# Performance work log

Measured on AMD Instinct MI355X. Metric: run time of the kernel, lower is better.

The kernel has to match this reference:

```python
import jax, jax.numpy as jnp
import numpy as np

KH, KW = 3, 3
STRIDE = 1
PAD = 1


def setup_inputs() -> dict:
    key = jax.random.key(0)
    kf, ko, kw_ = jax.random.split(key, 3)
    B, C, H, W = 4, 128, 96, 320
    Cout = 128
    features = jax.random.normal(kf, (B, C, H, W), dtype=jnp.float32)
    # perspective offsets in the original are O(offset_2d / D_RATIO) = O(2)
    offsets = jax.random.normal(ko, (B, 2 * KH * KW, H, W), dtype=jnp.float32) * 2.0
    weight = jax.random.normal(kw_, (Cout, C, KH, KW), dtype=jnp.float32) * (1.0 / np.sqrt(C * KH * KW))
    return {"features": features, "offsets": offsets, "weight": weight}


def _bilinear_sample(img, py, px):
    """img: [C,H,W]; py, px: [K,Ho,Wo] float sampling locations.
    Zero padding outside the image (torchvision deform_conv2d semantics).
    Returns [C,K,Ho,Wo]."""
    C, H, W = img.shape
    y0 = jnp.floor(py)
    x0 = jnp.floor(px)
    y1 = y0 + 1.0
    x1 = x0 + 1.0
    wy1 = py - y0
    wy0 = 1.0 - wy1
    wx1 = px - x0
    wx0 = 1.0 - wx1

    def gather(yy, xx):
        valid = (yy >= 0) & (yy <= H - 1) & (xx >= 0) & (xx <= W - 1)
        yi = jnp.clip(yy, 0, H - 1).astype(jnp.int32)
        xi = jnp.clip(xx, 0, W - 1).astype(jnp.int32)
        v = img[:, yi, xi]  # [C,K,Ho,Wo]
        return v * valid[None].astype(img.dtype)

    return (gather(y0, x0) * (wy0 * wx0)[None]
            + gather(y0, x1) * (wy0 * wx1)[None]
            + gather(y1, x0) * (wy1 * wx0)[None]
            + gather(y1, x1) * (wy1 * wx1)[None])


def deform_conv2d(x, offset, weight, stride=STRIDE, pad=PAD):
    B, C, H, W = x.shape
    Cout, Cin, kh, kw = weight.shape
    Ho = (H + 2 * pad - kh) // stride + 1
    Wo = (W + 2 * pad - kw) // stride + 1
    K = kh * kw
    # torchvision layout: channel 2k = dy, channel 2k+1 = dx, taps row-major
    off = offset.reshape(B, K, 2, Ho, Wo)
    ky, kx = jnp.meshgrid(jnp.arange(kh), jnp.arange(kw), indexing='ij')
    ky = ky.reshape(-1).astype(x.dtype)  # [K]
    kx = kx.reshape(-1).astype(x.dtype)
    hy = (jnp.arange(Ho) * stride - pad).astype(x.dtype)  # [Ho]
    wx = (jnp.arange(Wo) * stride - pad).astype(x.dtype)  # [Wo]
    base_y = ky[:, None, None] + hy[None, :, None]  # [K,Ho,1]
    base_x = kx[:, None, None] + wx[None, None, :]  # [K,1,Wo]
    py = base_y[None] + off[:, :, 0]  # [B,K,Ho,Wo]
    px = base_x[None] + off[:, :, 1]
    sampled = jax.vmap(_bilinear_sample)(x, py, px)  # [B,C,K,Ho,Wo]
    out = jnp.einsum('ok,bkn->bon',
                     weight.reshape(Cout, Cin * K),
                     sampled.reshape(B, Cin * K, Ho * Wo))
    return out.reshape(B, Cout, Ho, Wo)


def reference(features, offsets, weight):
    return deform_conv2d(features, offsets, weight)
```

## Files before the change

kernel.cpp:

```cpp
#include <hip/hip_runtime.h>
#include <hip/hip_fp16.h>

#define IH   96
#define IW   320
#define NB   4
#define CIN  128
#define COUT 128
#define NKP  9
#define HW   (IH*IW)

typedef float    f32x4 __attribute__((ext_vector_type(4)));
typedef _Float16 f16x8 __attribute__((ext_vector_type(8)));

__global__ __launch_bounds__(256) void k_transpose(const float* __restrict__ in,
                                                   unsigned* __restrict__ dst32) {
    __shared__ float tile[32][129];
    int bid = blockIdx.x;
    int xc = bid % 10;
    int by = bid / 10;
    int y = by % IH;
    int b = by / IH;
    int x0 = xc * 32;
    int tid = threadIdx.x;

    const float* src = in + (size_t)b * CIN * HW + (size_t)y * IW + x0;
#pragma unroll
    for (int i = 0; i < 16; ++i) {
        int idx = tid + 256 * i;
        int c = idx >> 5, xl = idx & 31;
        tile[xl][c] = src[(size_t)c * HW + xl];
    }
    __syncthreads();
    unsigned* d = dst32 + ((size_t)(b * IH + y) * IW + x0) * 64;
#pragma unroll
    for (int i = 0; i < 8; ++i) {
        int idx = tid + 256 * i;
        int c2 = idx & 63, xl = idx >> 6;
        __half2 p;
        p.x = __float2half(tile[xl][2 * c2]);
        p.y = __float2half(tile[xl][2 * c2 + 1]);
        d[xl * 64 + c2] = *(unsigned*)&p;
    }
}

__global__ __launch_bounds__(256) void k_prepack(const float* __restrict__ w,
                                                 _Float16* __restrict__ wb) {
    int idx = blockIdx.x * 256 + threadIdx.x;
    int kp = idx >> 14;
    int cout = (idx >> 7) & 127;
    int c = idx & 127;
    wb[idx] = (_Float16)w[(cout * CIN + c) * NKP + kp];
}

__global__ __launch_bounds__(256) void k_meta(const float* __restrict__ off,
                                              uint4* __restrict__ meta) {
    int idx = blockIdx.x * 256 + threadIdx.x;
    int wo = idx % IW;
    int t = idx / IW;
    int ho = t % IH;
    t /= IH;
    int kp = t % NKP;
    int b = t / NKP;

    float dy = off[((size_t)(b * 18 + 2 * kp) * IH + ho) * IW + wo];
    float dx = off[((size_t)(b * 18 + 2 * kp + 1) * IH + ho) * IW + wo];
    int ky = kp / 3, kx = kp - 3 * (kp / 3);
    float py = (float)(ho - 1 + ky) + dy;
    float px = (float)(wo - 1 + kx) + dx;
    float y0f = floorf(py), x0f = floorf(px);
    float wy1 = py - y0f, wx1 = px - x0f;
    float wy0 = 1.f - wy1, wx0 = 1.f - wx1;
    int y0 = (int)y0f, x0 = (int)x0f, y1 = y0 + 1, x1 = x0 + 1;
    wy0 = (y0 >= 0 && y0 < IH) ? wy0 : 0.f;
    wy1 = (y1 >= 0 && y1 < IH) ? wy1 : 0.f;
    wx0 = (x0 >= 0 && x0 < IW) ? wx0 : 0.f;
    wx1 = (x1 >= 0 && x1 < IW) ? wx1 : 0.f;
    int yc0 = min(max(y0, 0), IH - 1), yc1 = min(max(y1, 0), IH - 1);
    int xc0 = min(max(x0, 0), IW - 1), xc1 = min(max(x1, 0), IW - 1);
    unsigned r0 = (unsigned)((b * IH + yc0) * IW);
    unsigned r1 = (unsigned)((b * IH + yc1) * IW);

    auto pk = [](float w) {
        __half h = __float2half(w);
        __half2 p; p.x = h; p.y = h;
        return *(unsigned*)&p;
    };
    uint4 m0 = {pk(wy0 * wx0), pk(wy0 * wx1), pk(wy1 * wx0), pk(wy1 * wx1)};
    uint4 m1 = {(r0 + (unsigned)xc0) << 8, (r0 + (unsigned)xc1) << 8,
                (r1 + (unsigned)xc0) << 8, (r1 + (unsigned)xc1) << 8};
    meta[(size_t)idx * 2] = m0;
    meta[(size_t)idx * 2 + 1] = m1;
}

__global__ __launch_bounds__(256, 4) void k_main(const uint4* __restrict__ meta,
                                                 const char* __restrict__ fb,
                                                 const _Float16* __restrict__ wb,
                                                 float* __restrict__ out) {
    __shared__ unsigned colbuf[64 * 64];

    const int tid  = threadIdx.x;
    const int lane = tid & 63;
    const int wv   = tid >> 6;
    int bid = (blockIdx.x & 7) * 240 + (blockIdx.x >> 3);
    const int n0   = bid * 64;
    const int b    = n0 / HW;
    const int rem  = n0 - b * HW;
    const int ho   = rem / IW;
    const int wo0  = rem - ho * IW;
    const int lane4 = lane << 2;

    f32x4 acc[2][4];
#pragma unroll
    for (int mi = 0; mi < 2; ++mi)
#pragma unroll
        for (int nj = 0; nj < 4; ++nj)
            acc[mi][nj] = (f32x4){0.f, 0.f, 0.f, 0.f};

    for (int kp = 0; kp < NKP; ++kp) {
        const int itemBase = ((b * NKP + kp) * IH + ho) * IW + wo0;
#pragma unroll 4
        for (int i = 0; i < 16; ++i) {
            int p = (wv << 4) + i;
            int it = __builtin_amdgcn_readfirstlane(itemBase + p);
            uint4 mw = meta[(size_t)it * 2];
            uint4 ma = meta[(size_t)it * 2 + 1];
            __half2 u00 = *(const __half2*)(fb + ma.x + lane4);
            __half2 u01 = *(const __half2*)(fb + ma.y + lane4);
            __half2 u10 = *(const __half2*)(fb + ma.z + lane4);
            __half2 u11 = *(const __half2*)(fb + ma.w + lane4);
            __half2 s = __hmul2(*(const __half2*)&mw.x, u00);
            s = __hfma2(*(const __half2*)&mw.y, u01, s);
            s = __hfma2(*(const __half2*)&mw.z, u10, s);
            s = __hfma2(*(const __half2*)&mw.w, u11, s);
            colbuf[(p << 6) + (lane ^ ((p & 7) << 2))] = *(unsigned*)&s;
        }
        __syncthreads();

        const _Float16* wkbase =
            wb + (size_t)kp * COUT * CIN + (size_t)(wv * 32 + (lane & 15)) * CIN + 8 * (lane >> 4);
#pragma unroll
        for (int c0 = 0; c0 < CIN; c0 += 32) {
            f16x8 a0 = *(const f16x8*)(wkbase + c0);
            f16x8 a1 = *(const f16x8*)(wkbase + 16 * CIN + c0);
            int cb = (c0 >> 1) + 4 * (lane >> 4);
#pragma unroll
            for (int nj = 0; nj < 4; ++nj) {
                int pos = nj * 16 + (lane & 15);
                f16x8 bfr = *(const f16x8*)(&colbuf[(pos << 6) + (cb ^ ((pos & 7) << 2))]);
                acc[0][nj] = __builtin_amdgcn_mfma_f32_16x16x32_f16(a0, bfr, acc[0][nj], 0, 0, 0);
                acc[1][nj] = __builtin_amdgcn_mfma_f32_16x16x32_f16(a1, bfr, acc[1][nj], 0, 0, 0);
            }
        }
        __syncthreads();
    }

#pragma unroll
    for (int mi = 0; mi < 2; ++mi) {
#pragma unroll
        for (int nj = 0; nj < 4; ++nj) {
            int cout = wv * 32 + mi * 16 + ((lane >> 4) << 2);
            int wo = wo0 + nj * 16 + (lane & 15);
            float* op = out + ((size_t)(b * COUT + cout) * IH + ho) * IW + wo;
#pragma unroll
            for (int r = 0; r < 4; ++r)
                op[(size_t)r * HW] = acc[mi][nj][r];
        }
    }
}

extern "C" void kernel_launch(void* const* d_in, const int* in_sizes, int n_in,
                              void* d_out, int out_size, void* d_ws, size_t ws_size,
                              hipStream_t stream) {
    const float* features = (const float*)d_in[0];
    const float* offsets  = (const float*)d_in[1];
    const float* weight   = (const float*)d_in[2];
    float* out = (float*)d_out;

    unsigned*  nhwc = (unsigned*)d_ws;
    _Float16*  wbuf = (_Float16*)((char*)d_ws + (size_t)NB * HW * CIN * 2);
    uint4*     meta = (uint4*)((char*)d_ws + (size_t)NB * HW * CIN * 2 + 294912);

    hipLaunchKernelGGL(k_transpose, dim3(NB * IH * (IW / 32)), dim3(256), 0, stream, features, nhwc);
    hipLaunchKernelGGL(k_prepack, dim3(576), dim3(256), 0, stream, weight, wbuf);
    hipLaunchKernelGGL(k_meta, dim3(NB * NKP * IH * IW / 256), dim3(256), 0, stream, offsets, meta);
    hipLaunchKernelGGL(k_main, dim3((NB * HW) / 64), dim3(256), 0, stream,
                       meta, (const char*)nhwc, wbuf, out);
}
```

Baseline: 249.2 us.

## Double-buffer im2col gather against MFMA and merge preprocessing kernels

Merges the transpose, weight prepack and meta kernels into one launch that dispatches on block index. The main kernel gains a double-buffered LDS column buffer, so the bilinear gather for the next kernel tap is issued and interleaved with the MFMAs on the current tap, with one barrier per tap instead of two. Each block now handles two 64-pixel tiles in sequence, and the weights for a tap are loaded into registers up front. This is meant to hide gather latency and cut launch overhead, at the cost of more LDS and more registers, which may lower occupancy.

```diff
diff --git a/kernel.cpp b/kernel.cpp
--- a/kernel.cpp
+++ b/kernel.cpp
@@ -12,49 +12,53 @@
 typedef float    f32x4 __attribute__((ext_vector_type(4)));
 typedef _Float16 f16x8 __attribute__((ext_vector_type(8)));
 
-__global__ __launch_bounds__(256) void k_transpose(const float* __restrict__ in,
-                                                   unsigned* __restrict__ dst32) {
+__global__ __launch_bounds__(256) void k_pre(const float* __restrict__ feat,
+                                             const float* __restrict__ off,
+                                             const float* __restrict__ w,
+                                             unsigned* __restrict__ nhwc,
+                                             _Float16* __restrict__ wb,
+                                             uint4* __restrict__ meta) {
     __shared__ float tile[32][129];
     int bid = blockIdx.x;
-    int xc = bid % 10;
-    int by = bid / 10;
-    int y = by % IH;
-    int b = by / IH;
-    int x0 = xc * 32;
     int tid = threadIdx.x;
 
-    const float* src = in + (size_t)b * CIN * HW + (size_t)y * IW + x0;
-#pragma unroll
-    for (int i = 0; i < 16; ++i) {
-        int idx = tid + 256 * i;
-        int c = idx >> 5, xl = idx & 31;
-        tile[xl][c] = src[(size_t)c * HW + xl];
+    if (bid < 3840) {
+        int xc = bid % 10;
+        int by = bid / 10;
+        int y = by % IH;
+        int b = by / IH;
+        int x0 = xc * 32;
+        const float* src = feat + (size_t)b * CIN * HW + (size_t)y * IW + x0;
+#pragma unroll
+        for (int i = 0; i < 16; ++i) {
+            int idx = tid + 256 * i;
+            int c = idx >> 5, xl = idx & 31;
+            tile[xl][c] = src[(size_t)c * HW + xl];
+        }
+        __syncthreads();
+        unsigned* d = nhwc + ((size_t)(b * IH + y) * IW + x0) * 64;
+#pragma unroll
+        for (int i = 0; i < 8; ++i) {
+            int idx = tid + 256 * i;
+            int c2 = idx & 63, xl = idx >> 6;
+            __half2 p;
+            p.x = __float2half(tile[xl][2 * c2]);
+            p.y = __float2half(tile[xl][2 * c2 + 1]);
+            d[xl * 64 + c2] = *(unsigned*)&p;
+        }
+        return;
     }
-    __syncthreads();
-    unsigned* d = dst32 + ((size_t)(b * IH + y) * IW + x0) * 64;
-#pragma unroll
-    for (int i = 0; i < 8; ++i) {
-        int idx = tid + 256 * i;
-        int c2 = idx & 63, xl = idx >> 6;
-        __half2 p;
-        p.x = __float2half(tile[xl][2 * c2]);
-        p.y = __float2half(tile[xl][2 * c2 + 1]);
-        d[xl * 64 + c2] = *(unsigned*)&p;
+    bid -= 3840;
+    if (bid < 576) {
+        int idx = bid * 256 + tid;
+        int kp = idx >> 14;
+        int cout = (idx >> 7) & 127;
+        int c = idx & 127;
+        wb[idx] = (_Float16)w[(cout * CIN + c) * NKP + kp];
+        return;
     }
-}
-
-__global__ __launch_bounds__(256) void k_prepack(const float* __restrict__ w,
-                                                 _Float16* __restrict__ wb) {
-    int idx = blockIdx.x * 256 + threadIdx.x;
-    int kp = idx >> 14;
-    int cout = (idx >> 7) & 127;
-    int c = idx & 127;
-    wb[idx] = (_Float16)w[(cout * CIN + c) * NKP + kp];
-}
-
-__global__ __launch_bounds__(256) void k_meta(const float* __restrict__ off,
-                                              uint4* __restrict__ meta) {
-    int idx = blockIdx.x * 256 + threadIdx.x;
+    bid -= 576;
+    int idx = bid * 256 + tid;
     int wo = idx % IW;
     int t = idx / IW;
     int ho = t % IH;
@@ -79,9 +83,8 @@
     int xc0 = min(max(x0, 0), IW - 1), xc1 = min(max(x1, 0), IW - 1);
     unsigned r0 = (unsigned)((b * IH + yc0) * IW);
     unsigned r1 = (unsigned)((b * IH + yc1) * IW);
-
-    auto pk = [](float w) {
-        __half h = __float2half(w);
+    auto pk = [](float wgt) {
+        __half h = __float2half(wgt);
         __half2 p; p.x = h; p.y = h;
         return *(unsigned*)&p;
     };
@@ -96,74 +99,127 @@
                                                  const char* __restrict__ fb,
                                                  const _Float16* __restrict__ wb,
                                                  float* __restrict__ out) {
-    __shared__ unsigned colbuf[64 * 64];
+    __shared__ unsigned colbuf[2 * 64 * 64];
+    char* cb_ = (char*)colbuf;
 
     const int tid  = threadIdx.x;
     const int lane = tid & 63;
     const int wv   = tid >> 6;
-    int bid = (blockIdx.x & 7) * 240 + (blockIdx.x >> 3);
-    const int n0   = bid * 64;
-    const int b    = n0 / HW;
-    const int rem  = n0 - b * HW;
-    const int ho   = rem / IW;
-    const int wo0  = rem - ho * IW;
-    const int lane4 = lane << 2;
-
-    f32x4 acc[2][4];
-#pragma unroll
-    for (int mi = 0; mi < 2; ++mi)
-#pragma unroll
-        for (int nj = 0; nj < 4; ++nj)
-            acc[mi][nj] = (f32x4){0.f, 0.f, 0.f, 0.f};
-
-    for (int kp = 0; kp < NKP; ++kp) {
-        const int itemBase = ((b * NKP + kp) * IH + ho) * IW + wo0;
-#pragma unroll 4
-        for (int i = 0; i < 16; ++i) {
-            int p = (wv << 4) + i;
-            int it = __builtin_amdgcn_readfirstlane(itemBase + p);
-            uint4 mw = meta[(size_t)it * 2];
-            uint4 ma = meta[(size_t)it * 2 + 1];
-            __half2 u00 = *(const __half2*)(fb + ma.x + lane4);
-            __half2 u01 = *(const __half2*)(fb + ma.y + lane4);
-            __half2 u10 = *(const __half2*)(fb + ma.z + lane4);
-            __half2 u11 = *(const __half2*)(fb + ma.w + lane4);
-            __half2 s = __hmul2(*(const __half2*)&mw.x, u00);
-            s = __hfma2(*(const __half2*)&mw.y, u01, s);
-            s = __hfma2(*(const __half2*)&mw.z, u10, s);
-            s = __hfma2(*(const __half2*)&mw.w, u11, s);
-            colbuf[(p << 6) + (lane ^ ((p & 7) << 2))] = *(unsigned*)&s;
+    const int posl = lane & 15;
+    const int hi   = lane >> 4;
+    const int x    = (posl & 7) << 2;
+    const int vA   = (posl << 8) + (((4 * hi) ^ (x & 12)) << 2);
+    const int xe   = (x & 16) << 2;
+    const int xo   = xe ^ 64;
+    const int l4   = lane << 2;
+    const int wrb0 = l4 + (wv << 12);
+
+    int bid = (blockIdx.x & 7) * 120 + (blockIdx.x >> 3);
+    const int n0 = bid * 128;
+    const int b  = n0 / HW;
+    const int nrem0 = n0 - b * HW;
+
+    const int wvoff = (wv * 32 + posl) * CIN + 8 * hi;
+
+    for (int st = 0; st < 2; ++st) {
+        const int nrem = nrem0 + st * 64;
+        f32x4 acc[2][4];
+#pragma unroll
+        for (int mi = 0; mi < 2; ++mi)
+#pragma unroll
+            for (int nj = 0; nj < 4; ++nj)
+                acc[mi][nj] = (f32x4){0.f, 0.f, 0.f, 0.f};
+
+        {
+            const int itBase = (b * NKP + 0) * HW + nrem + wv * 16;
+#pragma unroll
+            for (int i = 0; i < 16; ++i) {
+                int it = __builtin_amdgcn_readfirstlane(itBase + i);
+                uint4 mw = meta[(size_t)it * 2];
+                uint4 ma = meta[(size_t)it * 2 + 1];
+                unsigned u0 = *(const unsigned*)(fb + ma.x + l4);
+                unsigned u1 = *(const unsigned*)(fb + ma.y + l4);
+                unsigned u2 = *(const unsigned*)(fb + ma.z + l4);
+                unsigned u3 = *(const unsigned*)(fb + ma.w + l4);
+                __half2 s = __hmul2(*(const __half2*)&mw.x, *(const __half2*)&u0);
+                s = __hfma2(*(const __half2*)&mw.y, *(const __half2*)&u1, s);
+                s = __hfma2(*(const __half2*)&mw.z, *(const __half2*)&u2, s);
+                s = __hfma2(*(const __half2*)&mw.w, *(const __half2*)&u3, s);
+                *(unsigned*)(cb_ + (wrb0 ^ ((i & 7) << 4)) + (i << 8)) = *(unsigned*)&s;
+            }
         }
         __syncthreads();
 
-        const _Float16* wkbase =
-            wb + (size_t)kp * COUT * CIN + (size_t)(wv * 32 + (lane & 15)) * CIN + 8 * (lane >> 4);
-#pragma unroll
-        for (int c0 = 0; c0 < CIN; c0 += 32) {
-            f16x8 a0 = *(const f16x8*)(wkbase + c0);
-            f16x8 a1 = *(const f16x8*)(wkbase + 16 * CIN + c0);
-            int cb = (c0 >> 1) + 4 * (lane >> 4);
+        for (int kp = 0; kp < NKP; ++kp) {
+            const int cur = kp & 1;
+            const int curB = cur << 14;
+            const int nxtB = curB ^ (1 << 14);
+            const int ave = vA + xe + curB;
+            const int avo = vA + xo + curB;
+            const int wrb = wrb0 + nxtB;
+            const int itBase = (b * NKP + (kp + 1)) * HW + nrem + wv * 16;
+            const bool more = (kp < NKP - 1);
+
+            const _Float16* wk0 = wb + (size_t)kp * COUT * CIN + wvoff;
+            const _Float16* wk1 = wk0 + 16 * CIN;
+            f16x8 wl[2][4];
+#pragma unroll
+            for (int g = 0; g < 4; ++g) {
+                wl[0][g] = *(const f16x8*)(wk0 + 32 * g);
+                wl[1][g] = *(const f16x8*)(wk1 + 32 * g);
+            }
+
+#pragma unroll
+            for (int q = 0; q < 4; ++q) {
+                uint4 mwv[4];
+                unsigned ug[4][4];
+                if (more) {
+#pragma unroll
+                    for (int i = 0; i < 4; ++i) {
+                        int it = __builtin_amdgcn_readfirstlane(itBase + q * 4 + i);
+                        mwv[i] = meta[(size_t)it * 2];
+                        uint4 ma = meta[(size_t)it * 2 + 1];
+                        ug[i][0] = *(const unsigned*)(fb + ma.x + l4);
+                        ug[i][1] = *(const unsigned*)(fb + ma.y + l4);
+                        ug[i][2] = *(const unsigned*)(fb + ma.z + l4);
+                        ug[i][3] = *(const unsigned*)(fb + ma.w + l4);
+                    }
+                }
+                {
+                    const int sel = (q & 1) ? avo : ave;
+                    const int himm = (q >> 1) << 7;
+#pragma unroll
+                    for (int nj = 0; nj < 4; ++nj) {
+                        f16x8 bf = *(const f16x8*)(cb_ + sel + ((nj << 12) + himm));
+                        acc[0][nj] = __builtin_amdgcn_mfma_f32_16x16x32_f16(wl[0][q], bf, acc[0][nj], 0, 0, 0);
+                        acc[1][nj] = __builtin_amdgcn_mfma_f32_16x16x32_f16(wl[1][q], bf, acc[1][nj], 0, 0, 0);
+                    }
+                }
+                if (more) {
+#pragma unroll
+                    for (int i = 0; i < 4; ++i) {
+                        __half2 s = __hmul2(*(const __half2*)&mwv[i].x, *(const __half2*)&ug[i][0]);
+                        s = __hfma2(*(const __half2*)&mwv[i].y, *(const __half2*)&ug[i][1], s);
+                        s = __hfma2(*(const __half2*)&mwv[i].z, *(const __half2*)&ug[i][2], s);
+                        s = __hfma2(*(const __half2*)&mwv[i].w, *(const __half2*)&ug[i][3], s);
+                        const int p = q * 4 + i;
+                        *(unsigned*)(cb_ + (wrb ^ ((p & 7) << 4)) + (p << 8)) = *(unsigned*)&s;
+                    }
+                }
+            }
+            __syncthreads();
+        }
+
+        float* obase = out + ((size_t)(b * COUT + wv * 32)) * HW + nrem;
+#pragma unroll
+        for (int mi = 0; mi < 2; ++mi) {
 #pragma unroll
             for (int nj = 0; nj < 4; ++nj) {
-                int pos = nj * 16 + (lane & 15);
-                f16x8 bfr = *(const f16x8*)(&colbuf[(pos << 6) + (cb ^ ((pos & 7) << 2))]);
-                acc[0][nj] = __builtin_amdgcn_mfma_f32_16x16x32_f16(a0, bfr, acc[0][nj], 0, 0, 0);
-                acc[1][nj] = __builtin_amdgcn_mfma_f32_16x16x32_f16(a1, bfr, acc[1][nj], 0, 0, 0);
-            }
-        }
-        __syncthreads();
-    }
-
-#pragma unroll
-    for (int mi = 0; mi < 2; ++mi) {
-#pragma unroll
-        for (int nj = 0; nj < 4; ++nj) {
-            int cout = wv * 32 + mi * 16 + ((lane >> 4) << 2);
-            int wo = wo0 + nj * 16 + (lane & 15);
-            float* op = out + ((size_t)(b * COUT + cout) * IH + ho) * IW + wo;
-#pragma unroll
-            for (int r = 0; r < 4; ++r)
-                op[(size_t)r * HW] = acc[mi][nj][r];
+                float* op = obase + (size_t)(mi * 16 + 4 * hi) * HW + nj * 16 + posl;
+#pragma unroll
+                for (int r = 0; r < 4; ++r)
+                    op[(size_t)r * HW] = acc[mi][nj][r];
+            }
         }
     }
 }
@@ -180,9 +236,8 @@
     _Float16*  wbuf = (_Float16*)((char*)d_ws + (size_t)NB * HW * CIN * 2);
     uint4*     meta = (uint4*)((char*)d_ws + (size_t)NB * HW * CIN * 2 + 294912);
 
-    hipLaunchKernelGGL(k_transpose, dim3(NB * IH * (IW / 32)), dim3(256), 0, stream, features, nhwc);
-    hipLaunchKernelGGL(k_prepack, dim3(576), dim3(256), 0, stream, weight, wbuf);
-    hipLaunchKernelGGL(k_meta, dim3(NB * NKP * IH * IW / 256), dim3(256), 0, stream, offsets, meta);
-    hipLaunchKernelGGL(k_main, dim3((NB * HW) / 64), dim3(256), 0, stream,
+    hipLaunchKernelGGL(k_pre, dim3(8736), dim3(256), 0, stream,
+                       features, offsets, weight, nhwc, wbuf, meta);
+    hipLaunchKernelGGL(k_main, dim3(960), dim3(256), 0, stream,
                        meta, (const char*)nhwc, wbuf, out);
 }
```

After: 268.7 us. 1.08x slower.

## Fuse sampling metadata into main kernel and merge transpose with weight prepack

Applied to the files above, without the earlier changes.

Removes the separate metadata kernel and its global buffer. Each block now computes bilinear indices and weights for its 64 positions directly from the offsets, double-buffered in shared memory and overlapped with the gather of the previous tap. The transpose and weight-prepack kernels are merged into one launch, and the metadata is packed more compactly (x1 encoded as a one-bit delta, fp16 weight pairs splatted at use). Occupancy hint rises to 6 blocks per SM. This cuts launches and global metadata traffic in exchange for extra ALU work and a partially idle wave inside the main kernel.

```diff
diff --git a/kernel.cpp b/kernel.cpp
--- a/kernel.cpp
+++ b/kernel.cpp
@@ -12,102 +12,103 @@
 typedef float    f32x4 __attribute__((ext_vector_type(4)));
 typedef _Float16 f16x8 __attribute__((ext_vector_type(8)));
 
-__global__ __launch_bounds__(256) void k_transpose(const float* __restrict__ in,
-                                                   unsigned* __restrict__ dst32) {
+__device__ __forceinline__ unsigned splat_lo(unsigned u) { return (u & 0xffffu) | (u << 16); }
+__device__ __forceinline__ unsigned splat_hi(unsigned u) { return (u >> 16) | (u & 0xffff0000u); }
+
+__global__ __launch_bounds__(256) void k_pre(const float* __restrict__ feat,
+                                             const float* __restrict__ w,
+                                             unsigned* __restrict__ nhwc,
+                                             _Float16* __restrict__ wb) {
     __shared__ float tile[32][129];
     int bid = blockIdx.x;
-    int xc = bid % 10;
-    int by = bid / 10;
-    int y = by % IH;
-    int b = by / IH;
-    int x0 = xc * 32;
     int tid = threadIdx.x;
 
-    const float* src = in + (size_t)b * CIN * HW + (size_t)y * IW + x0;
+    if (bid < 3840) {
+        int xc = bid % 10;
+        int by = bid / 10;
+        int y = by % IH;
+        int b = by / IH;
+        int x0 = xc * 32;
+        const float* src = feat + (size_t)b * CIN * HW + (size_t)y * IW + x0;
 #pragma unroll
-    for (int i = 0; i < 16; ++i) {
-        int idx = tid + 256 * i;
-        int c = idx >> 5, xl = idx & 31;
-        tile[xl][c] = src[(size_t)c * HW + xl];
+        for (int i = 0; i < 16; ++i) {
+            int idx = tid + 256 * i;
+            int c = idx >> 5, xl = idx & 31;
+            tile[xl][c] = src[(size_t)c * HW + xl];
+        }
+        __syncthreads();
+        unsigned* d = nhwc + ((size_t)(b * IH + y) * IW + x0) * 64;
+#pragma unroll
+        for (int i = 0; i < 8; ++i) {
+            int idx = tid + 256 * i;
+            int c2 = idx & 63, xl = idx >> 6;
+            __half2 p;
+            p.x = __float2half(tile[xl][2 * c2]);
+            p.y = __float2half(tile[xl][2 * c2 + 1]);
+            d[xl * 64 + c2] = *(unsigned*)&p;
+        }
+        return;
     }
-    __syncthreads();
-    unsigned* d = dst32 + ((size_t)(b * IH + y) * IW + x0) * 64;
-#pragma unroll
-    for (int i = 0; i < 8; ++i) {
-        int idx = tid + 256 * i;
-        int c2 = idx & 63, xl = idx >> 6;
-        __half2 p;
-        p.x = __float2half(tile[xl][2 * c2]);
-        p.y = __float2half(tile[xl][2 * c2 + 1]);
-        d[xl * 64 + c2] = *(unsigned*)&p;
-    }
-}
-
-__global__ __launch_bounds__(256) void k_prepack(const float* __restrict__ w,
-                                                 _Float16* __restrict__ wb) {
-    int idx = blockIdx.x * 256 + threadIdx.x;
+    bid -= 3840;
+    int idx = bid * 256 + tid;
     int kp = idx >> 14;
     int cout = (idx >> 7) & 127;
     int c = idx & 127;
     wb[idx] = (_Float16)w[(cout * CIN + c) * NKP + kp];
 }
 
-__global__ __launch_bounds__(256) void k_meta(const float* __restrict__ off,
-                                              uint4* __restrict__ meta) {
-    int idx = blockIdx.x * 256 + threadIdx.x;
-    int wo = idx % IW;
-    int t = idx / IW;
-    int ho = t % IH;
-    t /= IH;
-    int kp = t % NKP;
-    int b = t / NKP;
-
-    float dy = off[((size_t)(b * 18 + 2 * kp) * IH + ho) * IW + wo];
-    float dx = off[((size_t)(b * 18 + 2 * kp + 1) * IH + ho) * IW + wo];
-    int ky = kp / 3, kx = kp - 3 * (kp / 3);
-    float py = (float)(ho - 1 + ky) + dy;
-    float px = (float)(wo - 1 + kx) + dx;
-    float y0f = floorf(py), x0f = floorf(px);
-    float wy1 = py - y0f, wx1 = px - x0f;
-    float wy0 = 1.f - wy1, wx0 = 1.f - wx1;
-    int y0 = (int)y0f, x0 = (int)x0f, y1 = y0 + 1, x1 = x0 + 1;
-    wy0 = (y0 >= 0 && y0 < IH) ? wy0 : 0.f;
-    wy1 = (y1 >= 0 && y1 < IH) ? wy1 : 0.f;
-    wx0 = (x0 >= 0 && x0 < IW) ? wx0 : 0.f;
-    wx1 = (x1 >= 0 && x1 < IW) ? wx1 : 0.f;
-    int yc0 = min(max(y0, 0), IH - 1), yc1 = min(max(y1, 0), IH - 1);
-    int xc0 = min(max(x0, 0), IW - 1), xc1 = min(max(x1, 0), IW - 1);
-    unsigned r0 = (unsigned)((b * IH + yc0) * IW);
-    unsigned r1 = (unsigned)((b * IH + yc1) * IW);
-
-    auto pk = [](float w) {
-        __half h = __float2half(w);
-        __half2 p; p.x = h; p.y = h;
-        return *(unsigned*)&p;
-    };
-    uint4 m0 = {pk(wy0 * wx0), pk(wy0 * wx1), pk(wy1 * wx0), pk(wy1 * wx1)};
-    uint4 m1 = {(r0 + (unsigned)xc0) << 8, (r0 + (unsigned)xc1) << 8,
-                (r1 + (unsigned)xc0) << 8, (r1 + (unsigned)xc1) << 8};
-    meta[(size_t)idx * 2] = m0;
-    meta[(size_t)idx * 2 + 1] = m1;
-}
-
-__global__ __launch_bounds__(256, 4) void k_main(const uint4* __restrict__ meta,
+__global__ __launch_bounds__(256, 6) void k_main(const float* __restrict__ off,
                                                  const char* __restrict__ fb,
                                                  const _Float16* __restrict__ wb,
                                                  float* __restrict__ out) {
     __shared__ unsigned colbuf[64 * 64];
+    __shared__ uint4 metabuf[2][64];
 
     const int tid  = threadIdx.x;
     const int lane = tid & 63;
     const int wv   = tid >> 6;
+    const int posl = lane & 15;
+    const int hi   = lane >> 4;
+    const int l4   = lane << 2;
+
     int bid = (blockIdx.x & 7) * 240 + (blockIdx.x >> 3);
-    const int n0   = bid * 64;
-    const int b    = n0 / HW;
-    const int rem  = n0 - b * HW;
-    const int ho   = rem / IW;
-    const int wo0  = rem - ho * IW;
-    const int lane4 = lane << 2;
+    const int n0  = bid * 64;
+    const int b   = n0 / HW;
+    const int rem = n0 - b * HW;
+    const int ho  = rem / IW;
+    const int wo0 = rem - ho * IW;
+
+    const bool mlane = (lane < 16);
+    const int mp = wv * 16 + posl;
+    const int rowoff = ho * IW + wo0 + mp;
+
+    auto metacalc = [&](int k) {
+        if (!mlane) return;
+        const float* basep = off + (size_t)(b * 18 + 2 * k) * HW + rowoff;
+        float dy = basep[0];
+        float dx = basep[HW];
+        int ky = k / 3, kx = k - 3 * (k / 3);
+        float py = (float)(ho - 1 + ky) + dy;
+        float px = (float)(wo0 + mp - 1 + kx) + dx;
+        float y0f = floorf(py), x0f = floorf(px);
+        float wy1 = py - y0f, wx1 = px - x0f;
+        float wy0 = 1.f - wy1, wx0 = 1.f - wx1;
+        int y0 = (int)y0f, x0 = (int)x0f, y1 = y0 + 1, x1 = x0 + 1;
+        wy0 = (y0 >= 0 && y0 < IH) ? wy0 : 0.f;
+        wy1 = (y1 >= 0 && y1 < IH) ? wy1 : 0.f;
+        wx0 = (x0 >= 0 && x0 < IW) ? wx0 : 0.f;
+        wx1 = (x1 >= 0 && x1 < IW) ? wx1 : 0.f;
+        int yc0 = min(max(y0, 0), IH - 1), yc1 = min(max(y1, 0), IH - 1);
+        int xc0 = min(max(x0, 0), IW - 1), xc1 = min(max(x1, 0), IW - 1);
+        uint4 m;
+        m.x = ((unsigned)((b * IH + yc0) * IW + xc0) << 8) | (unsigned)(xc1 - xc0);
+        m.y = (unsigned)((b * IH + yc1) * IW + xc0) << 8;
+        __half2 wz; wz.x = __float2half(wy0 * wx0); wz.y = __float2half(wy0 * wx1);
+        __half2 ww; ww.x = __float2half(wy1 * wx0); ww.y = __float2half(wy1 * wx1);
+        m.z = *(unsigned*)&wz;
+        m.w = *(unsigned*)&ww;
+        metabuf[k & 1][mp] = m;
+    };
 
     f32x4 acc[2][4];
 #pragma unroll
@@ -116,36 +117,42 @@
         for (int nj = 0; nj < 4; ++nj)
             acc[mi][nj] = (f32x4){0.f, 0.f, 0.f, 0.f};
 
+    metacalc(0);
+    __syncthreads();
+
     for (int kp = 0; kp < NKP; ++kp) {
-        const int itemBase = ((b * NKP + kp) * IH + ho) * IW + wo0;
-#pragma unroll 4
+        const int cur = kp & 1;
+#pragma unroll
         for (int i = 0; i < 16; ++i) {
             int p = (wv << 4) + i;
-            int it = __builtin_amdgcn_readfirstlane(itemBase + p);
-            uint4 mw = meta[(size_t)it * 2];
-            uint4 ma = meta[(size_t)it * 2 + 1];
-            __half2 u00 = *(const __half2*)(fb + ma.x + lane4);
-            __half2 u01 = *(const __half2*)(fb + ma.y + lane4);
-            __half2 u10 = *(const __half2*)(fb + ma.z + lane4);
-            __half2 u11 = *(const __half2*)(fb + ma.w + lane4);
-            __half2 s = __hmul2(*(const __half2*)&mw.x, u00);
-            s = __hfma2(*(const __half2*)&mw.y, u01, s);
-            s = __hfma2(*(const __half2*)&mw.z, u10, s);
-            s = __hfma2(*(const __half2*)&mw.w, u11, s);
+            uint4 m = metabuf[cur][p];
+            unsigned d  = (m.x & 1u) << 8;
+            unsigned a00 = m.x & 0xffffff00u;
+            unsigned u00 = *(const unsigned*)(fb + a00 + l4);
+            unsigned u01 = *(const unsigned*)(fb + (a00 + d) + l4);
+            unsigned u10 = *(const unsigned*)(fb + m.y + l4);
+            unsigned u11 = *(const unsigned*)(fb + (m.y + d) + l4);
+            unsigned w00 = splat_lo(m.z), w01 = splat_hi(m.z);
+            unsigned w10 = splat_lo(m.w), w11 = splat_hi(m.w);
+            __half2 s = __hmul2(*(__half2*)&w00, *(__half2*)&u00);
+            s = __hfma2(*(__half2*)&w01, *(__half2*)&u01, s);
+            s = __hfma2(*(__half2*)&w10, *(__half2*)&u10, s);
+            s = __hfma2(*(__half2*)&w11, *(__half2*)&u11, s);
             colbuf[(p << 6) + (lane ^ ((p & 7) << 2))] = *(unsigned*)&s;
         }
+        if (kp < NKP - 1) metacalc(kp + 1);
         __syncthreads();
 
         const _Float16* wkbase =
-            wb + (size_t)kp * COUT * CIN + (size_t)(wv * 32 + (lane & 15)) * CIN + 8 * (lane >> 4);
+            wb + (size_t)kp * COUT * CIN + (size_t)(wv * 32 + posl) * CIN + 8 * hi;
 #pragma unroll
         for (int c0 = 0; c0 < CIN; c0 += 32) {
             f16x8 a0 = *(const f16x8*)(wkbase + c0);
             f16x8 a1 = *(const f16x8*)(wkbase + 16 * CIN + c0);
-            int cb = (c0 >> 1) + 4 * (lane >> 4);
+            int cb = (c0 >> 1) + 4 * hi;
 #pragma unroll
             for (int nj = 0; nj < 4; ++nj) {
-                int pos = nj * 16 + (lane & 15);
+                int pos = nj * 16 + posl;
                 f16x8 bfr = *(const f16x8*)(&colbuf[(pos << 6) + (cb ^ ((pos & 7) << 2))]);
                 acc[0][nj] = __builtin_amdgcn_mfma_f32_16x16x32_f16(a0, bfr, acc[0][nj], 0, 0, 0);
                 acc[1][nj] = __builtin_amdgcn_mfma_f32_16x16x32_f16(a1, bfr, acc[1][nj], 0, 0, 0);
@@ -158,8 +165,8 @@
     for (int mi = 0; mi < 2; ++mi) {
 #pragma unroll
         for (int nj = 0; nj < 4; ++nj) {
-            int cout = wv * 32 + mi * 16 + ((lane >> 4) << 2);
-            int wo = wo0 + nj * 16 + (lane & 15);
+            int cout = wv * 32 + mi * 16 + 4 * hi;
+            int wo = wo0 + nj * 16 + posl;
             float* op = out + ((size_t)(b * COUT + cout) * IH + ho) * IW + wo;
 #pragma unroll
             for (int r = 0; r < 4; ++r)
@@ -178,11 +185,9 @@
 
     unsigned*  nhwc = (unsigned*)d_ws;
     _Float16*  wbuf = (_Float16*)((char*)d_ws + (size_t)NB * HW * CIN * 2);
-    uint4*     meta = (uint4*)((char*)d_ws + (size_t)NB * HW * CIN * 2 + 294912);
 
-    hipLaunchKernelGGL(k_transpose, dim3(NB * IH * (IW / 32)), dim3(256), 0, stream, features, nhwc);
-    hipLaunchKernelGGL(k_prepack, dim3(576), dim3(256), 0, stream, weight, wbuf);
-    hipLaunchKernelGGL(k_meta, dim3(NB * NKP * IH * IW / 256), dim3(256), 0, stream, offsets, meta);
+    hipLaunchKernelGGL(k_pre, dim3(4416), dim3(256), 0, stream,
+                       features, weight, nhwc, wbuf);
     hipLaunchKernelGGL(k_main, dim3((NB * HW) / 64), dim3(256), 0, stream,
-                       meta, (const char*)nhwc, wbuf, out);
+                       offsets, (const char*)nhwc, wbuf, out);
 }
```

New measurement: 317.7 us. 1.27x slower.
